# Performance work log

Measured on AMD Instinct MI355X. Metric: run time of the kernel, lower is better.

The kernel has to match this reference:

```python
import jax, jax.numpy as jnp
import numpy as np

N_NODES = 100000
N_EDGES = 1600000
IN_DIM = 512
OUT_DIM = 128


def setup_inputs() -> dict:
    key = jax.random.key(0)
    ks = jax.random.split(key, 12)
    feat = jax.random.normal(ks[0], (N_NODES, IN_DIM), dtype=jnp.float32)
    shuf_feat = jax.random.normal(ks[1], (N_NODES, IN_DIM), dtype=jnp.float32)
    src1 = jax.random.randint(ks[2], (N_EDGES,), 0, N_NODES)
    dst1 = jax.random.randint(ks[3], (N_EDGES,), 0, N_NODES)
    src2 = jax.random.randint(ks[4], (N_EDGES,), 0, N_NODES)
    dst2 = jax.random.randint(ks[5], (N_EDGES,), 0, N_NODES)
    s = 1.0 / np.sqrt(IN_DIM)
    W1 = jax.random.uniform(ks[6], (IN_DIM, OUT_DIM), jnp.float32, -s, s)
    b1 = jnp.zeros((OUT_DIM,), jnp.float32)
    W2 = jax.random.uniform(ks[7], (IN_DIM, OUT_DIM), jnp.float32, -s, s)
    b2 = jnp.zeros((OUT_DIM,), jnp.float32)
    sb = 1.0 / np.sqrt(OUT_DIM)
    Wb = jax.random.uniform(ks[8], (OUT_DIM, OUT_DIM), jnp.float32, -sb, sb)
    bb = jax.random.uniform(ks[9], (), jnp.float32, -sb, sb)
    return {"feat": feat, "shuf_feat": shuf_feat, "src1": src1, "dst1": dst1,
            "src2": src2, "dst2": dst2, "W1": W1, "b1": b1, "W2": W2, "b2": b2,
            "Wb": Wb, "bb": bb}


def graph_conv(x, W, b, src, dst, n_nodes):
    # DGL GraphConv, norm='none', in_dim > out_dim: transform then sum-aggregate
    xw = x @ W                                    # [N, out_dim]
    agg = jax.ops.segment_sum(xw[src], dst, num_segments=n_nodes)
    return agg + b


def bilinear_score(h, c, Wb, bb):
    # h: [B, N, D], c: [B, D] -> [B, N]
    return jnp.einsum('bnd,de,be->bn', h, Wb, c) + bb


def reference(feat, shuf_feat, src1, dst1, src2, dst2, W1, b1, W2, b2, Wb, bb):
    n = feat.shape[0]
    h1 = graph_conv(feat, W1, b1, src1, dst1, n)
    h2 = graph_conv(feat, W2, b2, src2, dst2, n)
    c1 = jax.nn.sigmoid(jnp.mean(h1, axis=0, keepdims=True))  # [1, D]
    c2 = jax.nn.sigmoid(jnp.mean(h2, axis=0, keepdims=True))
    h3 = graph_conv(shuf_feat, W1, b1, src1, dst1, n)
    h4 = graph_conv(shuf_feat, W2, b2, src2, dst2, n)
    h1b, h2b, h3b, h4b = (h[None] for h in (h1, h2, h3, h4))  # [1, N, D]
    sc1 = bilinear_score(h2b, c1, Wb, bb)
    sc2 = bilinear_score(h1b, c2, Wb, bb)
    sc3 = bilinear_score(h4b, c1, Wb, bb)
    sc4 = bilinear_score(h3b, c2, Wb, bb)
    return jnp.concatenate((sc1, sc2, sc3, sc4), axis=1)  # [1, 4N]
```

## Files before the change

kernel.cpp:

```cpp
#include <hip/hip_runtime.h>
#include <math.h>

#define N_NODES 100000
#define N_EDGES 1600000
#define IN_DIM  512
#define OUT_DIM 128

#define OFF_S1    0
#define OFF_S2    512
#define OFF_M     1024
#define OFF_U     1280
#define OFF_WV    1536
#define OFF_ALPHA 2560
#define OFF_PA    4096
#define OFF_PB    204096
#define OFF_DEGR  404096
#define OFF_BUF   604096

#define P_SC   8192
#define NP_SC  13
#define P_D    16384
#define NP_D   7
#define WSUM_NBLK 1024

__global__ void k_zero(float* __restrict__ p, long n) {
    long i = (long)blockIdx.x * blockDim.x + threadIdx.x;
    long stride = (long)gridDim.x * blockDim.x;
    for (long j = i; j < n; j += stride) p[j] = 0.0f;
}

__global__ __launch_bounds__(512) void k_deg_b(const int* __restrict__ src1,
                                               const int* __restrict__ src2,
                                               int* __restrict__ degbuf, int Cd) {
    __shared__ int bins[P_D];
    const int part = blockIdx.x % NP_D;
    const int c    = blockIdx.x / NP_D;
    const int g    = blockIdx.y;
    const int tid  = threadIdx.x;
    const int base = part * P_D;
    const int4* srcv = (const int4*)(g ? src2 : src1);
    for (int i = tid; i < P_D; i += 512) bins[i] = 0;
    __syncthreads();
    const long E4 = N_EDGES / 4;
    const long s4 = ((long)c * E4) / Cd;
    const long e4 = ((long)(c + 1) * E4) / Cd;
    for (long i = s4 + tid; i < e4; i += 512) {
        int4 s = srcv[i];
        unsigned l0 = (unsigned)(s.x - base), l1 = (unsigned)(s.y - base);
        unsigned l2 = (unsigned)(s.z - base), l3 = (unsigned)(s.w - base);
        if (l0 < P_D) atomicAdd(&bins[l0], 1);
        if (l1 < P_D) atomicAdd(&bins[l1], 1);
        if (l2 < P_D) atomicAdd(&bins[l2], 1);
        if (l3 < P_D) atomicAdd(&bins[l3], 1);
    }
    __syncthreads();
    const int valid = min(P_D, N_NODES - base);
    int* o = degbuf + (size_t)c * 200000 + (size_t)g * 100000 + base;
    for (int l = tid; l < valid; l += 512) o[l] = bins[l];
}

__global__ void k_degred(const int* __restrict__ degbuf, int* __restrict__ degr, int Cd) {
    int j = blockIdx.x * blockDim.x + threadIdx.x;
    if (j < 200000) {
        int acc = 0;
        for (int c = 0; c < Cd; ++c) acc += degbuf[(size_t)c * 200000 + j];
        degr[j] = acc;
    }
}

__global__ __launch_bounds__(128) void k_wsum_p(const float* __restrict__ feat,
                                                const int* __restrict__ degr,
                                                float* __restrict__ pbuf) {
    const int t = threadIdx.x;
    const int k = 4 * t;
    const int chunk = (N_NODES + WSUM_NBLK - 1) / WSUM_NBLK;
    const int v0 = blockIdx.x * chunk;
    const int v1 = min(v0 + chunk, N_NODES);
    float4 a1 = {0.f, 0.f, 0.f, 0.f};
    float4 a2 = {0.f, 0.f, 0.f, 0.f};
    const float* fp = feat + (size_t)v0 * IN_DIM + k;
    int v = v0;
    for (; v + 4 <= v1; v += 4, fp += 4 * IN_DIM) {
        float4 f0 = *(const float4*)(fp);
        float4 f1 = *(const float4*)(fp + IN_DIM);
        float4 f2 = *(const float4*)(fp + 2 * IN_DIM);
        float4 f3 = *(const float4*)(fp + 3 * IN_DIM);
        float d10 = (float)degr[v],     d20 = (float)degr[100000 + v];
        float d11 = (float)degr[v + 1], d21 = (float)degr[100000 + v + 1];
        float d12 = (float)degr[v + 2], d22 = (float)degr[100000 + v + 2];
        float d13 = (float)degr[v + 3], d23 = (float)degr[100000 + v + 3];
        a1.x += d10 * f0.x + d11 * f1.x + d12 * f2.x + d13 * f3.x;
        a1.y += d10 * f0.y + d11 * f1.y + d12 * f2.y + d13 * f3.y;
        a1.z += d10 * f0.z + d11 * f1.z + d12 * f2.z + d13 * f3.z;
        a1.w += d10 * f0.w + d11 * f1.w + d12 * f2.w + d13 * f3.w;
        a2.x += d20 * f0.x + d21 * f1.x + d22 * f2.x + d23 * f3.x;
        a2.y += d20 * f0.y + d21 * f1.y + d22 * f2.y + d23 * f3.y;
        a2.z += d20 * f0.z + d21 * f1.z + d22 * f2.z + d23 * f3.z;
        a2.w += d20 * f0.w + d21 * f1.w + d22 * f2.w + d23 * f3.w;
    }
    for (; v < v1; ++v, fp += IN_DIM) {
        float4 f = *(const float4*)(fp);
        float d1 = (float)degr[v], d2 = (float)degr[100000 + v];
        a1.x += d1 * f.x; a1.y += d1 * f.y; a1.z += d1 * f.z; a1.w += d1 * f.w;
        a2.x += d2 * f.x; a2.y += d2 * f.y; a2.z += d2 * f.z; a2.w += d2 * f.w;
    }
    float* o = pbuf + (size_t)blockIdx.x * 1024;
    *(float4*)(o + k) = a1;
    *(float4*)(o + 512 + k) = a2;
}

__global__ void k_sred(const float* __restrict__ pbuf, float* __restrict__ s) {
    const int d = blockIdx.x * 256 + threadIdx.x;
    const int b0 = blockIdx.y * 64;
    float acc = 0.f;
#pragma unroll 8
    for (int b = 0; b < 64; ++b) acc += pbuf[(size_t)(b0 + b) * 1024 + d];
    atomicAdd(&s[d], acc);
}

__global__ void k_gemv_m(const float* __restrict__ ws, const float* __restrict__ W1,
                         const float* __restrict__ W2, float* __restrict__ m) {
    const int mat = blockIdx.y;
    const float* W = mat ? W2 : W1;
    const float* s = ws + (mat ? OFF_S2 : OFF_S1);
    const int t = threadIdx.x;
    const int k0 = blockIdx.x * 32;
    float acc = 0.f;
#pragma unroll 8
    for (int j = 0; j < 32; ++j)
        acc += s[k0 + j] * W[(k0 + j) * OUT_DIM + t];
    atomicAdd(&m[mat * OUT_DIM + t], acc);
}

__global__ void k_u(float* __restrict__ ws, const float* __restrict__ b1,
                    const float* __restrict__ b2, const float* __restrict__ Wb,
                    const float* __restrict__ bb) {
    __shared__ float c[OUT_DIM];
    __shared__ float red[128];
    const int mat = blockIdx.x;
    const int t = threadIdx.x;
    const float* b = mat ? b2 : b1;
    float mv = ws[OFF_M + mat * OUT_DIM + t] * (1.0f / N_NODES) + b[t];
    c[t] = 1.0f / (1.0f + expf(-mv));
    __syncthreads();
    float acc = 0.f;
    const float4* wr = (const float4*)(Wb + t * OUT_DIM);
#pragma unroll 8
    for (int j = 0; j < OUT_DIM / 4; ++j) {
        float4 w = wr[j];
        acc += w.x * c[4 * j] + w.y * c[4 * j + 1] + w.z * c[4 * j + 2] + w.w * c[4 * j + 3];
    }
    ws[OFF_U + mat * OUT_DIM + t] = acc;
    const float* bo = mat ? b1 : b2;
    red[t] = bo[t] * acc;
    __syncthreads();
    for (int s = 64; s > 0; s >>= 1) {
        if (t < s) red[t] += red[t + s];
        __syncthreads();
    }
    if (t == 0) ws[OFF_ALPHA + mat] = red[0] + bb[0];
}

__global__ void k_w(const float* __restrict__ ws, const float* __restrict__ W1,
                    const float* __restrict__ W2, float* __restrict__ wv) {
    const int wid = (blockIdx.x * blockDim.x + threadIdx.x) >> 6;
    const int lane = threadIdx.x & 63;
    const int mat = wid >> 9;
    const int k = wid & 511;
    const float* W = mat ? W2 : W1;
    const float* u = ws + OFF_U + (mat ? 0 : OUT_DIM);
    float2 w = *(const float2*)(W + k * OUT_DIM + 2 * lane);
    float2 uu = *(const float2*)(u + 2 * lane);
    float acc = w.x * uu.x + w.y * uu.y;
#pragma unroll
    for (int off = 32; off > 0; off >>= 1) acc += __shfl_down(acc, off);
    if (lane == 0) wv[mat * IN_DIM + k] = acc;
}

__device__ __forceinline__ float dot8(float4 a, float4 b, float4 wa, float4 wb) {
    return a.x * wa.x + a.y * wa.y + a.z * wa.z + a.w * wa.w
         + b.x * wb.x + b.y * wb.y + b.z * wb.z + b.w * wb.w;
}

__global__ void k_proj(const float* __restrict__ feat, const float* __restrict__ shuf,
                       const float* __restrict__ ws, float2* __restrict__ pA,
                       float2* __restrict__ pB) {
    const int lane = threadIdx.x & 63;
    const int gw = (blockIdx.x * blockDim.x + threadIdx.x) >> 6;
    const int nw = (gridDim.x * blockDim.x) >> 6;
    const int kA = 4 * lane;
    const int kB = 256 + 4 * lane;
    const float* wv = ws + OFF_WV;
    const float4 w12a = *(const float4*)(wv + kA);
    const float4 w12b = *(const float4*)(wv + kB);
    const float4 w21a = *(const float4*)(wv + IN_DIM + kA);
    const float4 w21b = *(const float4*)(wv + IN_DIM + kB);
    for (int v = gw; v < N_NODES; v += nw) {
        const float* rf = feat + (size_t)v * IN_DIM;
        float4 fa = *(const float4*)(rf + kA);
        float4 fb = *(const float4*)(rf + kB);
        const float* rs = shuf + (size_t)v * IN_DIM;
        float4 sa = *(const float4*)(rs + kA);
        float4 sb = *(const float4*)(rs + kB);
        float d12f = dot8(fa, fb, w12a, w12b);
        float d21f = dot8(fa, fb, w21a, w21b);
        float d12s = dot8(sa, sb, w12a, w12b);
        float d21s = dot8(sa, sb, w21a, w21b);
#pragma unroll
        for (int off = 32; off > 0; off >>= 1) {
            d12f += __shfl_down(d12f, off);
            d21f += __shfl_down(d21f, off);
            d12s += __shfl_down(d12s, off);
            d21s += __shfl_down(d21s, off);
        }
        if (lane == 0) {
            pA[v] = make_float2(d21f, d21s);
            pB[v] = make_float2(d12f, d12s);
        }
    }
}

__global__ __launch_bounds__(512) void k_sc_b(const int* __restrict__ src1,
                                              const int* __restrict__ dst1,
                                              const int* __restrict__ src2,
                                              const int* __restrict__ dst2,
                                              const float2* __restrict__ pA,
                                              const float2* __restrict__ pB,
                                              float* __restrict__ scbuf, int Cs) {
    __shared__ float bins[2 * P_SC];
    const int part = blockIdx.x % NP_SC;
    const int c    = blockIdx.x / NP_SC;
    const int g    = blockIdx.y;
    const int tid  = threadIdx.x;
    const int base = part * P_SC;
    const int4* dstv = (const int4*)(g ? dst2 : dst1);
    const int4* srcv = (const int4*)(g ? src2 : src1);
    const float2* tab = g ? pA : pB;
    for (int i = tid; i < 2 * P_SC; i += 512) bins[i] = 0.f;
    __syncthreads();
    const long E4 = N_EDGES / 4;
    const long s4 = ((long)c * E4) / Cs;
    const long e4 = ((long)(c + 1) * E4) / Cs;
    for (long i = s4 + tid; i < e4; i += 512) {
        int4 d = dstv[i];
        unsigned l0 = (unsigned)(d.x - base), l1 = (unsigned)(d.y - base);
        unsigned l2 = (unsigned)(d.z - base), l3 = (unsigned)(d.w - base);
        bool h0 = l0 < P_SC, h1 = l1 < P_SC, h2 = l2 < P_SC, h3 = l3 < P_SC;
        if (h0 | h1 | h2 | h3) {
            int4 s = srcv[i];
            if (h0) { float2 p = tab[s.x]; atomicAdd(&bins[l0], p.x); atomicAdd(&bins[P_SC + l0], p.y); }
            if (h1) { float2 p = tab[s.y]; atomicAdd(&bins[l1], p.x); atomicAdd(&bins[P_SC + l1], p.y); }
            if (h2) { float2 p = tab[s.z]; atomicAdd(&bins[l2], p.x); atomicAdd(&bins[P_SC + l2], p.y); }
            if (h3) { float2 p = tab[s.w]; atomicAdd(&bins[l3], p.x); atomicAdd(&bins[P_SC + l3], p.y); }
        }
    }
    __syncthreads();
    const int valid = min(P_SC, N_NODES - base);
    const int secA = g ? 0 : 1;
    const int secB = g ? 2 : 3;
    float* oA = scbuf + ((size_t)c * 4 + secA) * 100000 + base;
    float* oB = scbuf + ((size_t)c * 4 + secB) * 100000 + base;
    for (int l = tid; l < valid; l += 512) {
        oA[l] = bins[l];
        oB[l] = bins[P_SC + l];
    }
}

__global__ void k_final(const float* __restrict__ scbuf, const float* __restrict__ ws,
                        float* __restrict__ out, int Cs) {
    int i = blockIdx.x * blockDim.x + threadIdx.x;
    if (i < 4 * N_NODES) {
        int sec = i / N_NODES;
        int v = i - sec * N_NODES;
        float t = 0.f;
        for (int c = 0; c < Cs; ++c) t += scbuf[((size_t)c * 4 + sec) * 100000 + v];
        out[i] = ws[OFF_ALPHA + (sec & 1)] + t;
    }
}

__global__ void k_wsum_atomic(const float* __restrict__ feat, const int* __restrict__ degr,
                              float* __restrict__ s1, float* __restrict__ s2) {
    const int k = 4 * threadIdx.x;
    float4 a1 = {0.f, 0.f, 0.f, 0.f};
    float4 a2 = {0.f, 0.f, 0.f, 0.f};
    for (int v = blockIdx.x; v < N_NODES; v += gridDim.x) {
        float d1 = (float)degr[v];
        float d2 = (float)degr[100000 + v];
        float4 f = *reinterpret_cast<const float4*>(feat + (size_t)v * IN_DIM + k);
        a1.x += d1 * f.x; a1.y += d1 * f.y; a1.z += d1 * f.z; a1.w += d1 * f.w;
        a2.x += d2 * f.x; a2.y += d2 * f.y; a2.z += d2 * f.z; a2.w += d2 * f.w;
    }
    atomicAdd(&s1[k],     a1.x); atomicAdd(&s1[k + 1], a1.y);
    atomicAdd(&s1[k + 2], a1.z); atomicAdd(&s1[k + 3], a1.w);
    atomicAdd(&s2[k],     a2.x); atomicAdd(&s2[k + 1], a2.y);
    atomicAdd(&s2[k + 2], a2.z); atomicAdd(&s2[k + 3], a2.w);
}

__global__ void k_deg_direct(const int* __restrict__ src1, const int* __restrict__ src2,
                             int* __restrict__ degr) {
    int i = blockIdx.x * blockDim.x + threadIdx.x;
    if (i < N_EDGES) {
        atomicAdd(&degr[src1[i]], 1);
        atomicAdd(&degr[100000 + src2[i]], 1);
    }
}

__global__ void k_init(float* __restrict__ out, const float* __restrict__ ws) {
    int i = blockIdx.x * blockDim.x + threadIdx.x;
    if (i < 4 * N_NODES) {
        int sec = i / N_NODES;
        out[i] = ws[OFF_ALPHA + (sec & 1)];
    }
}

__global__ void k_scatter_direct(const int* __restrict__ src1, const int* __restrict__ dst1,
                                 const int* __restrict__ src2, const int* __restrict__ dst2,
                                 const float2* __restrict__ pA, const float2* __restrict__ pB,
                                 float* __restrict__ out) {
    int i = blockIdx.x * blockDim.x + threadIdx.x;
    if (i < N_EDGES) {
        int s1 = src1[i], d1 = dst1[i];
        int s2 = src2[i], d2 = dst2[i];
        float2 a = pA[s2];
        float2 b = pB[s1];
        atomicAdd(&out[d2],                 a.x);
        atomicAdd(&out[2 * N_NODES + d2],   a.y);
        atomicAdd(&out[N_NODES + d1],       b.x);
        atomicAdd(&out[3 * N_NODES + d1],   b.y);
    }
}

extern "C" void kernel_launch(void* const* d_in, const int* in_sizes, int n_in,
                              void* d_out, int out_size, void* d_ws, size_t ws_size,
                              hipStream_t stream) {
    const float* feat = (const float*)d_in[0];
    const float* shuf = (const float*)d_in[1];
    const int* src1 = (const int*)d_in[2];
    const int* dst1 = (const int*)d_in[3];
    const int* src2 = (const int*)d_in[4];
    const int* dst2 = (const int*)d_in[5];
    const float* W1 = (const float*)d_in[6];
    const float* b1 = (const float*)d_in[7];
    const float* W2 = (const float*)d_in[8];
    const float* b2 = (const float*)d_in[9];
    const float* Wb = (const float*)d_in[10];
    const float* bb = (const float*)d_in[11];
    float* out = (float*)d_out;

    float* wsf = (float*)d_ws;
    float2* pA = (float2*)(wsf + OFF_PA);
    float2* pB = (float2*)(wsf + OFF_PB);
    int* degr = (int*)(wsf + OFF_DEGR);

    long availf = (long)(ws_size / 4);
    long budget = availf - OFF_BUF;
    int Cd = 0, Cs = 0;
    if (budget >= 600000) {
        Cs = (int)((budget / 2) / 400000); if (Cs > 20) Cs = 20; if (Cs < 1) Cs = 1;
        Cd = (int)((budget - (long)Cs * 400000) / 200000); if (Cd > 36) Cd = 36; if (Cd < 1) Cd = 1;
    }
    const bool pb_ok = (budget >= 1048576);

    if (Cd >= 1) {
        int* degbuf = (int*)(wsf + OFF_BUF);
        float* pbuf = wsf + OFF_BUF;
        float* scbuf = wsf + OFF_BUF + (long)Cd * 200000;
        k_zero<<<2, 512, 0, stream>>>(wsf, 1280);
        k_deg_b<<<dim3(NP_D * Cd, 2), 512, 0, stream>>>(src1, src2, degbuf, Cd);
        k_degred<<<(200000 + 255) / 256, 256, 0, stream>>>(degbuf, degr, Cd);
        if (pb_ok) {
            k_wsum_p<<<WSUM_NBLK, 128, 0, stream>>>(feat, degr, pbuf);
            k_sred<<<dim3(4, 16), 256, 0, stream>>>(pbuf, wsf + OFF_S1);
        } else {
            k_wsum_atomic<<<2048, 128, 0, stream>>>(feat, degr, wsf + OFF_S1, wsf + OFF_S2);
        }
        k_gemv_m<<<dim3(16, 2), 128, 0, stream>>>(wsf, W1, W2, wsf + OFF_M);
        k_u<<<2, 128, 0, stream>>>(wsf, b1, b2, Wb, bb);
        k_w<<<256, 256, 0, stream>>>(wsf, W1, W2, wsf + OFF_WV);
        k_proj<<<8192, 256, 0, stream>>>(feat, shuf, wsf, pA, pB);
        k_sc_b<<<dim3(NP_SC * Cs, 2), 512, 0, stream>>>(src1, dst1, src2, dst2, pA, pB, scbuf, Cs);
        k_final<<<(4 * N_NODES + 255) / 256, 256, 0, stream>>>(scbuf, wsf, out, Cs);
    } else {
        k_zero<<<2, 512, 0, stream>>>(wsf, 1280);
        k_zero<<<256, 256, 0, stream>>>((float*)degr, 200000);
        k_deg_direct<<<(N_EDGES + 255) / 256, 256, 0, stream>>>(src1, src2, degr);
        k_wsum_atomic<<<2048, 128, 0, stream>>>(feat, degr, wsf + OFF_S1, wsf + OFF_S2);
        k_gemv_m<<<dim3(16, 2), 128, 0, stream>>>(wsf, W1, W2, wsf + OFF_M);
        k_u<<<2, 128, 0, stream>>>(wsf, b1, b2, Wb, bb);
        k_w<<<256, 256, 0, stream>>>(wsf, W1, W2, wsf + OFF_WV);
        k_proj<<<8192, 256, 0, stream>>>(feat, shuf, wsf, pA, pB);
        k_init<<<(4 * N_NODES + 255) / 256, 256, 0, stream>>>(out, wsf);
        k_scatter_direct<<<(N_EDGES + 255) / 256, 256, 0, stream>>>(src1, dst1, src2, dst2, pA, pB, out);
    }
}
```

Measured before the change: 656.8 us.

## Shrink histogram partitions, XCD-swizzle block mapping, and cap chunk counts

Halves the LDS bin partition sizes for the degree and score histogram kernels, which doubles the number of partitions. Cuts the edge-chunk counts to at most 16. It also flattens the grid and remaps block indices with an XCD-aware swizzle, so blocks working on the same edge chunk land on the same XCD and share its L2. Smaller LDS footprints should allow more resident blocks per CU. In exchange, each edge is scanned by more partitions, which adds redundant index reads.

```diff
diff --git a/kernel.cpp b/kernel.cpp
--- a/kernel.cpp
+++ b/kernel.cpp
@@ -17,11 +17,17 @@
 #define OFF_DEGR  404096
 #define OFF_BUF   604096
 
-#define P_SC   8192
-#define NP_SC  13
-#define P_D    16384
-#define NP_D   7
+#define P_SC   4096
+#define NP_SC  25
+#define P_D    8192
+#define NP_D   13
 #define WSUM_NBLK 1024
+
+__device__ __forceinline__ int xcd_swz(int bx, int nwg) {
+    const int q = nwg >> 3, r = nwg & 7;
+    const int x = bx & 7, i = bx >> 3;
+    return (x < r ? x * (q + 1) : r * (q + 1) + (x - r) * q) + i;
+}
 
 __global__ void k_zero(float* __restrict__ p, long n) {
     long i = (long)blockIdx.x * blockDim.x + threadIdx.x;
@@ -33,9 +39,12 @@
                                                const int* __restrict__ src2,
                                                int* __restrict__ degbuf, int Cd) {
     __shared__ int bins[P_D];
-    const int part = blockIdx.x % NP_D;
-    const int c    = blockIdx.x / NP_D;
-    const int g    = blockIdx.y;
+    const int nwg  = NP_D * Cd * 2;
+    const int l    = xcd_swz(blockIdx.x, nwg);
+    const int part = l % NP_D;
+    const int grp  = l / NP_D;
+    const int c    = grp % Cd;
+    const int g    = grp / Cd;
     const int tid  = threadIdx.x;
     const int base = part * P_D;
     const int4* srcv = (const int4*)(g ? src2 : src1);
@@ -44,6 +53,7 @@
     const long E4 = N_EDGES / 4;
     const long s4 = ((long)c * E4) / Cd;
     const long e4 = ((long)(c + 1) * E4) / Cd;
+#pragma unroll 2
     for (long i = s4 + tid; i < e4; i += 512) {
         int4 s = srcv[i];
         unsigned l0 = (unsigned)(s.x - base), l1 = (unsigned)(s.y - base);
@@ -56,7 +66,7 @@
     __syncthreads();
     const int valid = min(P_D, N_NODES - base);
     int* o = degbuf + (size_t)c * 200000 + (size_t)g * 100000 + base;
-    for (int l = tid; l < valid; l += 512) o[l] = bins[l];
+    for (int li = tid; li < valid; li += 512) o[li] = bins[li];
 }
 
 __global__ void k_degred(const int* __restrict__ degbuf, int* __restrict__ degr, int Cd) {
@@ -228,9 +238,12 @@
                                               const float2* __restrict__ pB,
                                               float* __restrict__ scbuf, int Cs) {
     __shared__ float bins[2 * P_SC];
-    const int part = blockIdx.x % NP_SC;
-    const int c    = blockIdx.x / NP_SC;
-    const int g    = blockIdx.y;
+    const int nwg  = NP_SC * Cs * 2;
+    const int l    = xcd_swz(blockIdx.x, nwg);
+    const int part = l % NP_SC;
+    const int grp  = l / NP_SC;
+    const int c    = grp % Cs;
+    const int g    = grp / Cs;
     const int tid  = threadIdx.x;
     const int base = part * P_SC;
     const int4* dstv = (const int4*)(g ? dst2 : dst1);
@@ -241,6 +254,7 @@
     const long E4 = N_EDGES / 4;
     const long s4 = ((long)c * E4) / Cs;
     const long e4 = ((long)(c + 1) * E4) / Cs;
+#pragma unroll 2
     for (long i = s4 + tid; i < e4; i += 512) {
         int4 d = dstv[i];
         unsigned l0 = (unsigned)(d.x - base), l1 = (unsigned)(d.y - base);
@@ -260,9 +274,9 @@
     const int secB = g ? 2 : 3;
     float* oA = scbuf + ((size_t)c * 4 + secA) * 100000 + base;
     float* oB = scbuf + ((size_t)c * 4 + secB) * 100000 + base;
-    for (int l = tid; l < valid; l += 512) {
-        oA[l] = bins[l];
-        oB[l] = bins[P_SC + l];
+    for (int li = tid; li < valid; li += 512) {
+        oA[li] = bins[li];
+        oB[li] = bins[P_SC + li];
     }
 }
 
@@ -356,8 +370,8 @@
     long budget = availf - OFF_BUF;
     int Cd = 0, Cs = 0;
     if (budget >= 600000) {
-        Cs = (int)((budget / 2) / 400000); if (Cs > 20) Cs = 20; if (Cs < 1) Cs = 1;
-        Cd = (int)((budget - (long)Cs * 400000) / 200000); if (Cd > 36) Cd = 36; if (Cd < 1) Cd = 1;
+        Cs = (int)((budget / 2) / 400000); if (Cs > 16) Cs = 16; if (Cs < 1) Cs = 1;
+        Cd = (int)((budget - (long)Cs * 400000) / 200000); if (Cd > 16) Cd = 16; if (Cd < 1) Cd = 1;
     }
     const bool pb_ok = (budget >= 1048576);
 
@@ -366,7 +380,7 @@
         float* pbuf = wsf + OFF_BUF;
         float* scbuf = wsf + OFF_BUF + (long)Cd * 200000;
         k_zero<<<2, 512, 0, stream>>>(wsf, 1280);
-        k_deg_b<<<dim3(NP_D * Cd, 2), 512, 0, stream>>>(src1, src2, degbuf, Cd);
+        k_deg_b<<<NP_D * Cd * 2, 512, 0, stream>>>(src1, src2, degbuf, Cd);
         k_degred<<<(200000 + 255) / 256, 256, 0, stream>>>(degbuf, degr, Cd);
         if (pb_ok) {
             k_wsum_p<<<WSUM_NBLK, 128, 0, stream>>>(feat, degr, pbuf);
@@ -378,7 +392,7 @@
         k_u<<<2, 128, 0, stream>>>(wsf, b1, b2, Wb, bb);
         k_w<<<256, 256, 0, stream>>>(wsf, W1, W2, wsf + OFF_WV);
         k_proj<<<8192, 256, 0, stream>>>(feat, shuf, wsf, pA, pB);
-        k_sc_b<<<dim3(NP_SC * Cs, 2), 512, 0, stream>>>(src1, dst1, src2, dst2, pA, pB, scbuf, Cs);
+        k_sc_b<<<NP_SC * Cs * 2, 512, 0, stream>>>(src1, dst1, src2, dst2, pA, pB, scbuf, Cs);
         k_final<<<(4 * N_NODES + 255) / 256, 256, 0, stream>>>(scbuf, wsf, out, Cs);
     } else {
         k_zero<<<2, 512, 0, stream>>>(wsf, 1280);
```

Measured after the change: 615.4 us. 1.07x faster.
